# Kernel optimization log

Hardware: AMD Instinct MI355X
Metric: run time of the kernel (lower is better)

The kernel has to match this reference:

```python
import jax, jax.numpy as jnp
import numpy as np

B, L, D = 2, 2048, 2048
H, KV = 32, 8
HD = D // H          # 64
REP = H // KV        # 4


def setup_inputs() -> dict:
    key = jax.random.key(0)
    ks = jax.random.split(key, 6)
    x = jax.random.normal(ks[0], (B, L, D), dtype=jnp.float32)
    # weights stored [in, out] (transpose of torch Linear weight), scaled for stability
    wq = jax.random.normal(ks[1], (D, H * HD), dtype=jnp.float32) * 0.02
    wk = jax.random.normal(ks[2], (D, KV * HD), dtype=jnp.float32) * 0.02
    wv = jax.random.normal(ks[3], (D, KV * HD), dtype=jnp.float32) * 0.02
    wo = jax.random.normal(ks[4], (H * HD, D), dtype=jnp.float32) * 0.02
    # RoPE frequencies: freqs_cis = exp(i * pos * theta), theta_j = 10000^{-2j/HD}
    inv_freq = 1.0 / (10000.0 ** (jnp.arange(0, HD, 2, dtype=jnp.float32) / HD))  # [HD/2]
    angles = jnp.arange(L, dtype=jnp.float32)[:, None] * inv_freq[None, :]        # [L, HD/2]
    freqs_cos = jnp.cos(angles)
    freqs_sin = jnp.sin(angles)
    # additive causal mask [L, L] (prefill from start_pos=0)
    mask = jnp.where(jnp.tril(jnp.ones((L, L), dtype=bool)), 0.0, -jnp.inf).astype(jnp.float32)
    return {"x": x, "start_pos": 0, "freqs_cos": freqs_cos, "freqs_sin": freqs_sin,
            "mask": mask, "wq": wq, "wk": wk, "wv": wv, "wo": wo}


def _apply_rope(t, cos, sin):
    # t: [B, L, h, HD]; cos/sin: [L, HD/2] -> broadcast [1, L, 1, HD/2]
    tp = t.reshape(*t.shape[:-1], HD // 2, 2)
    a, b = tp[..., 0], tp[..., 1]
    c = cos[None, :, None, :]
    s = sin[None, :, None, :]
    ra = a * c - b * s
    rb = a * s + b * c
    return jnp.stack([ra, rb], axis=-1).reshape(t.shape)


def reference(x, start_pos, freqs_cos, freqs_sin, mask, wq, wk, wv, wo):
    xq = jnp.einsum('bld,de->ble', x, wq).reshape(B, L, H, HD)
    xk = jnp.einsum('bld,de->ble', x, wk).reshape(B, L, KV, HD)
    xv = jnp.einsum('bld,de->ble', x, wv).reshape(B, L, KV, HD)
    xq = _apply_rope(xq, freqs_cos, freqs_sin)
    xk = _apply_rope(xk, freqs_cos, freqs_sin)
    # (cache write of xk/xv is a dead side effect in the torch module; omitted)
    # GQA: query head (g*REP + r) attends to kv head g  == repeat_interleave semantics
    q = xq.transpose(0, 2, 1, 3).reshape(B, KV, REP, L, HD)  # [B,KV,REP,L,HD]
    k = xk.transpose(0, 2, 1, 3)                              # [B,KV,L,HD]
    v = xv.transpose(0, 2, 1, 3)
    scale = 1.0 / jnp.sqrt(jnp.float32(HD))
    scores = jnp.einsum('bgrld,bgmd->bgrlm', q, k) * scale + mask  # [B,KV,REP,L,L]
    attn = jax.nn.softmax(scores, axis=-1)
    out = jnp.einsum('bgrlm,bgmd->bgrld', attn, v)            # [B,KV,REP,L,HD]
    out = out.reshape(B, H, L, HD).transpose(0, 2, 1, 3).reshape(B, L, H * HD)
    return jnp.einsum('ble,ed->bld', out, wo)
```

## Files before the change

kernel.cpp:

```cpp
#include <hip/hip_runtime.h>
#include <hip/hip_bf16.h>
#include <math.h>

typedef __bf16 bf16_t;
typedef __bf16 bf16x8 __attribute__((ext_vector_type(8)));
typedef __bf16 bf16x4 __attribute__((ext_vector_type(4)));
typedef __bf16 bf16x2 __attribute__((ext_vector_type(2)));
typedef float  f32x4  __attribute__((ext_vector_type(4)));
typedef int    i32x4  __attribute__((ext_vector_type(4)));

#define B_  2
#define L_  2048
#define D_  2048
#define H_  32
#define KV_ 8
#define HD_ 64

static __device__ __forceinline__ void gload_lds16(const bf16_t* g, void* l)
{
    __builtin_amdgcn_global_load_lds(
        (const __attribute__((address_space(1))) void*)g,
        (__attribute__((address_space(3))) void*)l, 16, 0, 0);
}

static __device__ __forceinline__ int packbf(float a, float b)
{
    bf16x2 t; t[0] = (bf16_t)a; t[1] = (bf16_t)b;
    return __builtin_bit_cast(int, t);
}

__global__ void cast_f32_bf16(const float4* __restrict__ in,
                              bf16x4* __restrict__ out, int n4)
{
    const int i = blockIdx.x * 256 + threadIdx.x;
    if (i >= n4) return;
    const float4 v = in[i];
    bf16x4 o;
    o[0] = (bf16_t)v.x; o[1] = (bf16_t)v.y; o[2] = (bf16_t)v.z; o[3] = (bf16_t)v.w;
    out[i] = o;
}

template <typename InT>
__global__ void transpose_cast(const InT* __restrict__ in, bf16_t* __restrict__ out,
                               int R, int C)
{
    __shared__ bf16_t tile[32][33];
    const int bx = blockIdx.x * 32, by = blockIdx.y * 32;
    in  += (size_t)blockIdx.z * R * C;
    out += (size_t)blockIdx.z * R * C;
    const int tx = threadIdx.x, ty = threadIdx.y;
#pragma unroll
    for (int i = ty; i < 32; i += 8)
        tile[i][tx] = (bf16_t)(float)in[(size_t)(by + i) * C + bx + tx];
    __syncthreads();
#pragma unroll
    for (int i = ty; i < 32; i += 8)
        out[(size_t)(bx + i) * R + by + tx] = tile[tx][i];
}

template <typename OutT>
__global__ __launch_bounds__(256) void gemm_tn(
    const bf16_t* __restrict__ A,
    const bf16_t* __restrict__ BT,
    OutT* __restrict__ C,
    int M, int N, int K)
{
    __shared__ __attribute__((aligned(16))) bf16_t As[128 * 32];
    __shared__ __attribute__((aligned(16))) bf16_t Bs[128 * 32];

    const int m0   = blockIdx.y * 128;
    const int n0   = blockIdx.x * 128;
    const int tid  = threadIdx.x;
    const int wave = tid >> 6;
    const int lane = tid & 63;
    const int quad = lane >> 4;
    const int l16  = lane & 15;
    const int wm   = (wave & 1) * 64;
    const int wn   = (wave >> 1) * 64;
    const int sr   = tid >> 2;
    const int sc   = (tid & 3) * 8;

    f32x4 acc[4][4];
    const f32x4 zf = {0.f, 0.f, 0.f, 0.f};
#pragma unroll
    for (int i = 0; i < 4; i++)
#pragma unroll
        for (int j = 0; j < 4; j++) acc[i][j] = zf;

    const bf16_t* ag = A  + (size_t)(m0 + sr) * K + sc;
    const bf16_t* bg = BT + (size_t)(n0 + sr) * K + sc;
    bf16_t* asl = As + tid * 8;
    bf16_t* bsl = Bs + tid * 8;

    for (int k0 = 0; k0 < K; k0 += 32) {
        gload_lds16(ag + k0,                  asl);
        gload_lds16(ag + (size_t)64 * K + k0, asl + 2048);
        gload_lds16(bg + k0,                  bsl);
        gload_lds16(bg + (size_t)64 * K + k0, bsl + 2048);
        __syncthreads();

        bf16x8 af[4], bfr[4];
#pragma unroll
        for (int i = 0; i < 4; i++)
            af[i] = *(const bf16x8*)(&As[(wm + i * 16 + l16) * 32 + quad * 8]);
#pragma unroll
        for (int i = 0; i < 4; i++)
            bfr[i] = *(const bf16x8*)(&Bs[(wn + i * 16 + l16) * 32 + quad * 8]);

#pragma unroll
        for (int mi = 0; mi < 4; mi++)
#pragma unroll
            for (int ni = 0; ni < 4; ni++)
                acc[mi][ni] = __builtin_amdgcn_mfma_f32_16x16x32_bf16(
                    af[mi], bfr[ni], acc[mi][ni], 0, 0, 0);
        __syncthreads();
    }

#pragma unroll
    for (int mi = 0; mi < 4; mi++)
#pragma unroll
        for (int ni = 0; ni < 4; ni++)
#pragma unroll
            for (int r = 0; r < 4; r++) {
                const int row = m0 + wm + mi * 16 + quad * 4 + r;
                const int col = n0 + wn + ni * 16 + l16;
                C[(size_t)row * N + col] = (OutT)acc[mi][ni][r];
            }
}

__global__ __launch_bounds__(256) void gemm_qkv(
    const bf16_t* __restrict__ A,
    const bf16_t* __restrict__ BT,
    bf16_t* __restrict__ Qb, bf16_t* __restrict__ Kb, bf16_t* __restrict__ Vb,
    int K)
{
    __shared__ __attribute__((aligned(16))) bf16_t As[128 * 32];
    __shared__ __attribute__((aligned(16))) bf16_t Bs[128 * 32];

    const int m0   = blockIdx.y * 128;
    const int n0   = blockIdx.x * 128;
    const int tid  = threadIdx.x;
    const int wave = tid >> 6;
    const int lane = tid & 63;
    const int quad = lane >> 4;
    const int l16  = lane & 15;
    const int wm   = (wave & 1) * 64;
    const int wn   = (wave >> 1) * 64;
    const int sr   = tid >> 2;
    const int sc   = (tid & 3) * 8;

    f32x4 acc[4][4];
    const f32x4 zf = {0.f, 0.f, 0.f, 0.f};
#pragma unroll
    for (int i = 0; i < 4; i++)
#pragma unroll
        for (int j = 0; j < 4; j++) acc[i][j] = zf;

    const bf16_t* ag = A  + (size_t)(m0 + sr) * K + sc;
    const bf16_t* bg = BT + (size_t)(n0 + sr) * K + sc;
    bf16_t* asl = As + tid * 8;
    bf16_t* bsl = Bs + tid * 8;

    for (int k0 = 0; k0 < K; k0 += 32) {
        gload_lds16(ag + k0,                  asl);
        gload_lds16(ag + (size_t)64 * K + k0, asl + 2048);
        gload_lds16(bg + k0,                  bsl);
        gload_lds16(bg + (size_t)64 * K + k0, bsl + 2048);
        __syncthreads();

        bf16x8 af[4], bfr[4];
#pragma unroll
        for (int i = 0; i < 4; i++)
            af[i] = *(const bf16x8*)(&As[(wm + i * 16 + l16) * 32 + quad * 8]);
#pragma unroll
        for (int i = 0; i < 4; i++)
            bfr[i] = *(const bf16x8*)(&Bs[(wn + i * 16 + l16) * 32 + quad * 8]);

#pragma unroll
        for (int mi = 0; mi < 4; mi++)
#pragma unroll
            for (int ni = 0; ni < 4; ni++)
                acc[mi][ni] = __builtin_amdgcn_mfma_f32_16x16x32_bf16(
                    af[mi], bfr[ni], acc[mi][ni], 0, 0, 0);
        __syncthreads();
    }

    bf16_t* Cb; int ldc, coff;
    if (n0 < 2048)      { Cb = Qb; ldc = 2048; coff = 0; }
    else if (n0 < 2560) { Cb = Kb; ldc = 512;  coff = 2048; }
    else                { Cb = Vb; ldc = 512;  coff = 2560; }

#pragma unroll
    for (int mi = 0; mi < 4; mi++)
#pragma unroll
        for (int ni = 0; ni < 4; ni++)
#pragma unroll
            for (int r = 0; r < 4; r++) {
                const int row = m0 + wm + mi * 16 + quad * 4 + r;
                const int col = n0 + wn + ni * 16 + l16 - coff;
                Cb[(size_t)row * ldc + col] = (bf16_t)acc[mi][ni][r];
            }
}

__global__ void rope_k(bf16_t* __restrict__ T, const float* __restrict__ fc,
                       const float* __restrict__ fs, int nheads, int total)
{
    const int idx = blockIdx.x * 256 + threadIdx.x;
    if (idx >= total) return;
    const int i  = idx & 31;
    const int t  = idx >> 5;
    const int h  = t % nheads;
    const int bl = t / nheads;
    const int l  = bl & (L_ - 1);
    const float c = fc[l * 32 + i];
    const float s = fs[l * 32 + i];
    const size_t off = ((size_t)bl * nheads + h) * 64 + 2 * i;
    const float a  = (float)T[off];
    const float b2 = (float)T[off + 1];
    T[off]     = (bf16_t)(a * c - b2 * s);
    T[off + 1] = (bf16_t)(a * s + b2 * c);
}

__global__ __launch_bounds__(256, 2) void attn_k(
    const bf16_t* __restrict__ Q,
    const bf16_t* __restrict__ Kc,
    const bf16_t* __restrict__ VT,
    bf16_t* __restrict__ Ob)
{
    __shared__ __attribute__((aligned(16))) char LDS[65536];
    float* OL = (float*)LDS;
    float* LR = (float*)(LDS + 17408);

    const int tid  = threadIdx.x;
    const int wave = tid >> 6;
    const int lane = tid & 63;
    const int quad = lane >> 4;
    const int l16  = lane & 15;
    const int c    = blockIdx.x;
    const int bh   = blockIdx.y;
    const int bb   = bh >> 5;
    const int h    = bh & 31;
    const int kvh  = h >> 2;
    const size_t bbL = (size_t)bb * L_;

    const bf16_t* Kg  = Kc + (bbL + (tid >> 2)) * (KV_ * HD_) + kvh * HD_ + (tid & 3) * 8;
    const bf16_t* Vg  = VT + (size_t)(bb * KV_ + kvh) * HD_ * L_ + (size_t)(tid >> 2) * L_ + (tid & 3) * 8;
    const f32x4 zf = {0.f, 0.f, 0.f, 0.f};

    for (int half = 0; half < 2; ++half) {
        const int j     = half ? c : 31 - c;
        const int qbase = j * 64;
        const int nkt   = (j + 2) >> 1;

        bf16x8 qf[4][2];
#pragma unroll
        for (int qt = 0; qt < 4; qt++) {
            const bf16_t* qrow = Q + ((bbL + qbase + qt * 16 + l16) * H_ + h) * HD_;
#pragma unroll
            for (int cc = 0; cc < 2; cc++) {
                bf16x8 v = *(const bf16x8*)(qrow + cc * 32 + quad * 8);
#pragma unroll
                for (int i = 0; i < 8; i++) v[i] = (bf16_t)((float)v[i] * 0.125f);
                qf[qt][cc] = v;
            }
        }

        f32x4 acc[4][4];
#pragma unroll
        for (int mt = 0; mt < 4; mt++)
#pragma unroll
            for (int qt = 0; qt < 4; qt++) acc[mt][qt] = zf;
        float lacc[4] = {0.f, 0.f, 0.f, 0.f};

        {
            char* kb = LDS;
#pragma unroll
            for (int cc = 0; cc < 2; cc++)
#pragma unroll
                for (int hh = 0; hh < 2; hh++)
                    gload_lds16(Kg + (size_t)(hh * 64) * (KV_ * HD_) + cc * 32,
                                kb + cc * 8192 + hh * 4096 + tid * 16);
#pragma unroll
            for (int kc = 0; kc < 4; kc++)
                gload_lds16(Vg + kc * 32, kb + 16384 + kc * 4096 + tid * 16);
        }

        for (int kt = 0; kt < nkt; kt++) {
            __syncthreads();

            if (kt + 1 < nkt) {
                char* kb = LDS + ((kt + 1) & 1) * 32768;
                const size_t ko = (size_t)(kt + 1) * 128;
#pragma unroll
                for (int cc = 0; cc < 2; cc++)
#pragma unroll
                    for (int hh = 0; hh < 2; hh++)
                        gload_lds16(Kg + (ko + hh * 64) * (KV_ * HD_) + cc * 32,
                                    kb + cc * 8192 + hh * 4096 + tid * 16);
#pragma unroll
                for (int kc = 0; kc < 4; kc++)
                    gload_lds16(Vg + ko + kc * 32, kb + 16384 + kc * 4096 + tid * 16);
            }

            const char* Kld = LDS + (kt & 1) * 32768;
            const char* Vld = Kld + 16384;

            bf16x8 kf[2][2];
#pragma unroll
            for (int t = 0; t < 2; t++)
#pragma unroll
                for (int cc = 0; cc < 2; cc++)
                    kf[t][cc] = *(const bf16x8*)(Kld + cc * 8192 +
                        (wave * 32 + t * 16 + l16) * 64 + quad * 16);

            f32x4 st[2][4];
#pragma unroll
            for (int t = 0; t < 2; t++)
#pragma unroll
                for (int qt = 0; qt < 4; qt++) {
                    f32x4 s = __builtin_amdgcn_mfma_f32_16x16x32_bf16(
                        kf[t][0], qf[qt][0], zf, 0, 0, 0);
                    st[t][qt] = __builtin_amdgcn_mfma_f32_16x16x32_bf16(
                        kf[t][1], qf[qt][1], s, 0, 0, 0);
                }

            bf16x8 vf[4];
#pragma unroll
            for (int mt = 0; mt < 4; mt++)
                vf[mt] = *(const bf16x8*)(Vld + wave * 4096 +
                    (mt * 16 + l16) * 64 + quad * 16);

            if (kt == nkt - 1) {
                const int kq = kt * 128 + wave * 32 + quad * 4 - qbase - l16;
#pragma unroll
                for (int t = 0; t < 2; t++)
#pragma unroll
                    for (int qt = 0; qt < 4; qt++)
#pragma unroll
                        for (int r = 0; r < 4; r++)
                            st[t][qt][r] = (kq + t * 16 - qt * 16 + r <= 0)
                                         ? st[t][qt][r] : -__builtin_inff();
            }

            int pk[2][4][2];
#pragma unroll
            for (int t = 0; t < 2; t++)
#pragma unroll
                for (int qt = 0; qt < 4; qt++) {
                    const float e0 = __expf(st[t][qt][0]);
                    const float e1 = __expf(st[t][qt][1]);
                    const float e2 = __expf(st[t][qt][2]);
                    const float e3 = __expf(st[t][qt][3]);
                    lacc[qt] += (e0 + e1) + (e2 + e3);
                    pk[t][qt][0] = packbf(e0, e1);
                    pk[t][qt][1] = packbf(e2, e3);
                }

            const int s1 = ((quad & 1) * 2) * 16 + l16;
            const int s2 = s1 + 16;
            const bool hi = quad >= 2;
#pragma unroll
            for (int qt = 0; qt < 4; qt++) {
                const int a0 = __shfl(pk[0][qt][0], s1);
                const int a1 = __shfl(pk[0][qt][1], s1);
                const int b0 = __shfl(pk[1][qt][0], s1);
                const int b1 = __shfl(pk[1][qt][1], s1);
                const int c0 = __shfl(pk[0][qt][0], s2);
                const int c1 = __shfl(pk[0][qt][1], s2);
                const int d0 = __shfl(pk[1][qt][0], s2);
                const int d1 = __shfl(pk[1][qt][1], s2);
                i32x4 bi;
                bi[0] = hi ? b0 : a0;
                bi[1] = hi ? b1 : a1;
                bi[2] = hi ? d0 : c0;
                bi[3] = hi ? d1 : c1;
                const bf16x8 pb = __builtin_bit_cast(bf16x8, bi);
#pragma unroll
                for (int mt = 0; mt < 4; mt++)
                    acc[mt][qt] = __builtin_amdgcn_mfma_f32_16x16x32_bf16(
                        vf[mt], pb, acc[mt][qt], 0, 0, 0);
            }
        }

        float lw[4];
#pragma unroll
        for (int qt = 0; qt < 4; qt++) {
            float v = lacc[qt];
            v += __shfl_xor(v, 16);
            v += __shfl_xor(v, 32);
            lw[qt] = v;
        }

        __syncthreads();

        if (quad == 0)
#pragma unroll
            for (int qt = 0; qt < 4; qt++)
                LR[(wave * 4 + qt) * 16 + l16] = lw[qt];

#pragma unroll
        for (int p = 0; p < 4; p++) {
#pragma unroll
            for (int qt = 0; qt < 4; qt++) {
                if (((qt - wave) & 3) == p) {
#pragma unroll
                    for (int mt = 0; mt < 4; mt++) {
                        float* a = OL + (qt * 16 + l16) * 68 + mt * 16 + quad * 4;
                        if (p == 0) *(f32x4*)a = acc[mt][qt];
                        else        *(f32x4*)a = *(f32x4*)a + acc[mt][qt];
                    }
                }
            }
            __syncthreads();
        }

        const float ls = LR[(0 * 4 + wave) * 16 + l16] + LR[(1 * 4 + wave) * 16 + l16]
                       + LR[(2 * 4 + wave) * 16 + l16] + LR[(3 * 4 + wave) * 16 + l16];
        const float inv = 1.f / ls;
        bf16_t* orow = Ob + ((bbL + qbase + wave * 16 + l16) * H_ + h) * HD_;
#pragma unroll
        for (int j2 = 0; j2 < 4; j2++) {
            const f32x4 v = *(const f32x4*)(OL + (wave * 16 + l16) * 68 + quad * 16 + j2 * 4);
            bf16x4 o;
#pragma unroll
            for (int i = 0; i < 4; i++) o[i] = (bf16_t)(v[i] * inv);
            *(bf16x4*)(orow + quad * 16 + j2 * 4) = o;
        }
        __syncthreads();
    }
}

extern "C" void kernel_launch(void* const* d_in, const int* in_sizes, int n_in,
                              void* d_out, int out_size, void* d_ws, size_t ws_size,
                              hipStream_t stream)
{
    (void)in_sizes; (void)n_in; (void)out_size; (void)ws_size;
    const float* xf = (const float*)d_in[0];
    const float* fc = (const float*)d_in[2];
    const float* fs = (const float*)d_in[3];
    const float* wq = (const float*)d_in[5];
    const float* wk = (const float*)d_in[6];
    const float* wv = (const float*)d_in[7];
    const float* wo = (const float*)d_in[8];
    float* out = (float*)d_out;

    char* ws = (char*)d_ws;
    bf16_t* xb   = (bf16_t*)(ws);
    bf16_t* Qb   = (bf16_t*)(ws + (16ull << 20));
    bf16_t* Kb   = (bf16_t*)(ws + (32ull << 20));
    bf16_t* Vb   = (bf16_t*)(ws + (36ull << 20));
    bf16_t* VTb  = (bf16_t*)(ws + (40ull << 20));
    bf16_t* Oa   = (bf16_t*)(ws + (44ull << 20));
    bf16_t* Wqkv = (bf16_t*)(ws + (60ull << 20));
    bf16_t* WoT  = (bf16_t*)(ws + (72ull << 20));

    cast_f32_bf16<<<8192, 256, 0, stream>>>((const float4*)xf, (bf16x4*)xb,
                                            B_ * L_ * D_ / 4);

    const dim3 tb(32, 8);
    transpose_cast<float><<<dim3(64, 64, 1), tb, 0, stream>>>(wq, Wqkv, 2048, 2048);
    transpose_cast<float><<<dim3(16, 64, 1), tb, 0, stream>>>(wk, Wqkv + 2048ull * 2048, 2048, 512);
    transpose_cast<float><<<dim3(16, 64, 1), tb, 0, stream>>>(wv, Wqkv + 2560ull * 2048, 2048, 512);
    transpose_cast<float><<<dim3(64, 64, 1), tb, 0, stream>>>(wo, WoT, 2048, 2048);

    gemm_qkv<<<dim3(24, 32), 256, 0, stream>>>(xb, Wqkv, Qb, Kb, Vb, 2048);

    rope_k<<<16384, 256, 0, stream>>>(Qb, fc, fs, 32, B_ * L_ * 32 * 32);
    rope_k<<<4096, 256, 0, stream>>>(Kb, fc, fs, 8, B_ * L_ * 8 * 32);

    transpose_cast<bf16_t><<<dim3(16, 64, 2), tb, 0, stream>>>(Vb, VTb, 2048, 512);

    attn_k<<<dim3(16, 64), 256, 0, stream>>>(Qb, Kb, VTb, Oa);

    gemm_tn<float><<<dim3(16, 32), 256, 0, stream>>>(Oa, WoT, out, 4096, 2048, 2048);
}
```

Before: 366.8 us.

## Vectorize RoPE, swizzle attention LDS layout, and raise MFMA wave priority

The RoPE kernel now handles eight bf16 elements per thread with 16-byte loads and stores instead of one pair per thread, so far fewer threads and memory transactions are needed. The attention kernel XOR-swizzles the column chunk used when K/V tiles are written into LDS and applies the same swizzle when fragments are read back, to cut LDS bank conflicts. It also wraps the MFMA sections in s_setprio to favour waves issuing matrix ops. The swizzle has to match exactly between the global-to-LDS load mapping and the reads, or the results will be wrong.

```diff
diff --git a/kernel.cpp b/kernel.cpp
--- a/kernel.cpp
+++ b/kernel.cpp
@@ -203,22 +203,30 @@
 }
 
 __global__ void rope_k(bf16_t* __restrict__ T, const float* __restrict__ fc,
-                       const float* __restrict__ fs, int nheads, int total)
+                       const float* __restrict__ fs, int nheads, int total8)
 {
     const int idx = blockIdx.x * 256 + threadIdx.x;
-    if (idx >= total) return;
-    const int i  = idx & 31;
-    const int t  = idx >> 5;
+    if (idx >= total8) return;
+    const int g  = idx & 7;
+    const int t  = idx >> 3;
     const int h  = t % nheads;
     const int bl = t / nheads;
     const int l  = bl & (L_ - 1);
-    const float c = fc[l * 32 + i];
-    const float s = fs[l * 32 + i];
-    const size_t off = ((size_t)bl * nheads + h) * 64 + 2 * i;
-    const float a  = (float)T[off];
-    const float b2 = (float)T[off + 1];
-    T[off]     = (bf16_t)(a * c - b2 * s);
-    T[off + 1] = (bf16_t)(a * s + b2 * c);
+    const float4 c4 = *(const float4*)(fc + l * 32 + g * 4);
+    const float4 s4 = *(const float4*)(fs + l * 32 + g * 4);
+    const size_t off = ((size_t)bl * nheads + h) * 64 + g * 8;
+    const bf16x8 v = *(const bf16x8*)(T + off);
+    const float cc[4] = {c4.x, c4.y, c4.z, c4.w};
+    const float ss[4] = {s4.x, s4.y, s4.z, s4.w};
+    bf16x8 o;
+#pragma unroll
+    for (int p = 0; p < 4; p++) {
+        const float a  = (float)v[2 * p];
+        const float b2 = (float)v[2 * p + 1];
+        o[2 * p]     = (bf16_t)(a * cc[p] - b2 * ss[p]);
+        o[2 * p + 1] = (bf16_t)(a * ss[p] + b2 * cc[p]);
+    }
+    *(bf16x8*)(T + off) = o;
 }
 
 __global__ __launch_bounds__(256, 2) void attn_k(
@@ -243,8 +251,11 @@
     const int kvh  = h >> 2;
     const size_t bbL = (size_t)bb * L_;
 
-    const bf16_t* Kg  = Kc + (bbL + (tid >> 2)) * (KV_ * HD_) + kvh * HD_ + (tid & 3) * 8;
-    const bf16_t* Vg  = VT + (size_t)(bb * KV_ + kvh) * HD_ * L_ + (size_t)(tid >> 2) * L_ + (tid & 3) * 8;
+    const int scol = (((tid & 3) ^ ((tid >> 3) & 3)) * 8);
+    const int sw16 = ((l16 >> 1) & 3) * 16;
+
+    const bf16_t* Kg  = Kc + (bbL + (tid >> 2)) * (KV_ * HD_) + kvh * HD_ + scol;
+    const bf16_t* Vg  = VT + (size_t)(bb * KV_ + kvh) * HD_ * L_ + (size_t)(tid >> 2) * L_ + scol;
     const f32x4 zf = {0.f, 0.f, 0.f, 0.f};
 
     for (int half = 0; half < 2; ++half) {
@@ -311,9 +322,10 @@
 #pragma unroll
                 for (int cc = 0; cc < 2; cc++)
                     kf[t][cc] = *(const bf16x8*)(Kld + cc * 8192 +
-                        (wave * 32 + t * 16 + l16) * 64 + quad * 16);
+                        (wave * 32 + t * 16 + l16) * 64 + ((quad * 16) ^ sw16));
 
             f32x4 st[2][4];
+            __builtin_amdgcn_s_setprio(1);
 #pragma unroll
             for (int t = 0; t < 2; t++)
 #pragma unroll
@@ -323,12 +335,13 @@
                     st[t][qt] = __builtin_amdgcn_mfma_f32_16x16x32_bf16(
                         kf[t][1], qf[qt][1], s, 0, 0, 0);
                 }
+            __builtin_amdgcn_s_setprio(0);
 
             bf16x8 vf[4];
 #pragma unroll
             for (int mt = 0; mt < 4; mt++)
                 vf[mt] = *(const bf16x8*)(Vld + wave * 4096 +
-                    (mt * 16 + l16) * 64 + quad * 16);
+                    (mt * 16 + l16) * 64 + ((quad * 16) ^ sw16));
 
             if (kt == nkt - 1) {
                 const int kq = kt * 128 + wave * 32 + quad * 4 - qbase - l16;
@@ -375,10 +388,12 @@
                 bi[2] = hi ? d0 : c0;
                 bi[3] = hi ? d1 : c1;
                 const bf16x8 pb = __builtin_bit_cast(bf16x8, bi);
+                __builtin_amdgcn_s_setprio(1);
 #pragma unroll
                 for (int mt = 0; mt < 4; mt++)
                     acc[mt][qt] = __builtin_amdgcn_mfma_f32_16x16x32_bf16(
                         vf[mt], pb, acc[mt][qt], 0, 0, 0);
+                __builtin_amdgcn_s_setprio(0);
             }
         }
 
@@ -465,8 +480,8 @@
 
     gemm_qkv<<<dim3(24, 32), 256, 0, stream>>>(xb, Wqkv, Qb, Kb, Vb, 2048);
 
-    rope_k<<<16384, 256, 0, stream>>>(Qb, fc, fs, 32, B_ * L_ * 32 * 32);
-    rope_k<<<4096, 256, 0, stream>>>(Kb, fc, fs, 8, B_ * L_ * 8 * 32);
+    rope_k<<<4096, 256, 0, stream>>>(Qb, fc, fs, 32, B_ * L_ * 32 * 8);
+    rope_k<<<1024, 256, 0, stream>>>(Kb, fc, fs, 8, B_ * L_ * 8 * 8);
 
     transpose_cast<bf16_t><<<dim3(16, 64, 2), tb, 0, stream>>>(Vb, VTb, 2048, 512);
 
```

After: 367.3 us. About the same (+0.1%).
